# Optimization experiments

Hardware: AMD Instinct MI355X
Metric: run time of the kernel (lower is better)

The kernel has to match this reference:

```python
import jax, jax.numpy as jnp
import numpy as np

N = 100000
E = 1600000
D_IN = 128
D_H = 128
D_OUT = 128
K = 2
EPS = 0.1


def setup_inputs() -> dict:
    key = jax.random.key(0)
    ks = jax.random.split(key, 10)
    x = jax.random.normal(ks[0], (N, D_IN), dtype=jnp.float32)
    edge_index = jax.random.randint(ks[1], (2, E), 0, N, dtype=jnp.int64)
    # parameters (scaled like torch default inits, small uniform)
    def lin(k, fan_in, shape):
        bound = 1.0 / np.sqrt(fan_in)
        return jax.random.uniform(k, shape, jnp.float32, -bound, bound)
    emb_w = lin(ks[2], D_IN, (D_IN, D_H))
    emb_b = lin(ks[3], D_IN, (D_H,))
    # TAGConv: K+1 linears (no bias) + one output bias
    conv_ws = jnp.stack([lin(ks[4 + i], D_H, (D_H, D_H)) for i in range(K + 1)])
    conv_b = lin(ks[7], D_H, (D_H,))
    ro_w = lin(ks[8], D_H, (D_H, D_OUT))
    ro_b = lin(ks[9], D_H, (D_OUT,))
    return {
        "x": x, "edge_index": edge_index, "delta_t": 4,
        "emb_w": emb_w, "emb_b": emb_b,
        "conv_ws": conv_ws, "conv_b": conv_b,
        "ro_w": ro_w, "ro_b": ro_b,
    }


def _tagconv(h, src, dst, norm, conv_ws, conv_b):
    """PyG TAGConv: out = sum_k W_k (A_hat^k h) + b, A_hat = D^-1/2 A D^-1/2 (no self loops)."""
    out = h @ conv_ws[0]
    xk = h
    for k in range(1, K + 1):
        msg = norm[:, None] * xk[src]            # [E, D_H] gather
        xk = jax.ops.segment_sum(msg, dst, num_segments=h.shape[0])  # scatter-add
        out = out + xk @ conv_ws[k]
    return out + conv_b


def reference(x, edge_index, delta_t, emb_w, emb_b, conv_ws, conv_b, ro_w, ro_b):
    src = edge_index[0]
    dst = edge_index[1]
    n = x.shape[0]
    # gcn_norm without self loops: deg over targets of unit edge weights
    deg = jnp.zeros((n,), jnp.float32).at[dst].add(1.0)
    dinv = jnp.where(deg > 0, jax.lax.rsqrt(jnp.maximum(deg, 1.0)), 0.0)
    norm = dinv[src] * dinv[dst]                 # [E]

    h = x @ emb_w + emb_b
    h_middle = h
    for _ in range(int(delta_t)):
        conv = _tagconv(h, src, dst, norm, conv_ws, conv_b)
        h_middle = h + 0.5 * EPS * jnp.tanh(conv)
        conv_mid = _tagconv(h_middle, src, dst, norm, conv_ws, conv_b)
        h = h + EPS * jnp.tanh(conv_mid)
    y = h_middle @ ro_w + ro_b
    return (y, h_middle)
```

## Files before the change

kernel.cpp:

```cpp
#include <hip/hip_runtime.h>
#include <hip/hip_bf16.h>

#define NN 100000
#define EE 1600000
#define DD 128
#define EPSc 0.1f
#define NBK 256
#define BKDIV 391
#define BKCAP 7168

typedef unsigned short bfu;
typedef __attribute__((ext_vector_type(8))) short short8;
typedef __attribute__((ext_vector_type(4))) float f32x4;
typedef __attribute__((ext_vector_type(2))) float f32x2;

__device__ __forceinline__ float bf2f(bfu s) {
    union { unsigned u; float f; } c; c.u = ((unsigned)s) << 16; return c.f;
}
__device__ __forceinline__ bfu f2bf(float f) {
    union { float f; unsigned u; } c; c.f = f;
    unsigned u = c.u + 0x7fffu + ((c.u >> 16) & 1u);
    return (bfu)(u >> 16);
}
__device__ __forceinline__ unsigned pk8(float a, float b, float c, float d) {
    int r = 0;
    r = __builtin_amdgcn_cvt_pk_fp8_f32(a, b, r, false);
    r = __builtin_amdgcn_cvt_pk_fp8_f32(c, d, r, true);
    return (unsigned)r;
}
__device__ __forceinline__ unsigned char enc8(float a) {
    return (unsigned char)(__builtin_amdgcn_cvt_pk_fp8_f32(a, a, 0, false) & 0xFF);
}
__device__ __forceinline__ short8 e8bf(uint2 u) {
    f32x2 p0 = __builtin_amdgcn_cvt_pk_f32_fp8((int)u.x, false);
    f32x2 p1 = __builtin_amdgcn_cvt_pk_f32_fp8((int)u.x, true);
    f32x2 p2 = __builtin_amdgcn_cvt_pk_f32_fp8((int)u.y, false);
    f32x2 p3 = __builtin_amdgcn_cvt_pk_f32_fp8((int)u.y, true);
    short8 s;
    s[0] = (short)f2bf(p0[0]); s[1] = (short)f2bf(p0[1]);
    s[2] = (short)f2bf(p1[0]); s[3] = (short)f2bf(p1[1]);
    s[4] = (short)f2bf(p2[0]); s[5] = (short)f2bf(p2[1]);
    s[6] = (short)f2bf(p3[0]); s[7] = (short)f2bf(p3[1]);
    return s;
}
__device__ __forceinline__ float ftanh(float x) {
    float xc = fminf(fmaxf(x, -9.0f), 9.0f);
    float e = __expf(2.0f * xc);
    return (e - 1.0f) * __builtin_amdgcn_rcpf(e + 1.0f);
}


__global__ __launch_bounds__(256) void count_deg_kernel(const int* __restrict__ dst,
                                                        int* __restrict__ ideg, int e_cnt) {
    int e = blockIdx.x * 256 + threadIdx.x;
    if (e < e_cnt) atomicAdd(&ideg[dst[e]], 1);
}

__global__ __launch_bounds__(256) void dinv_kernel(const int* __restrict__ ideg,
                                                   float* __restrict__ dinv, int n) {
    int i = blockIdx.x * 256 + threadIdx.x;
    if (i < n) {
        int d = ideg[i];
        dinv[i] = (d > 0) ? rsqrtf((float)d) : 0.0f;
    }
}

__global__ __launch_bounds__(256) void partial_sum_kernel(const int* __restrict__ ideg,
                                                          int* __restrict__ partials, int n) {
    __shared__ int sm[256];
    int i = blockIdx.x * 256 + threadIdx.x;
    sm[threadIdx.x] = (i < n) ? ideg[i] : 0;
    __syncthreads();
    for (int off = 128; off > 0; off >>= 1) {
        if ((int)threadIdx.x < off) sm[threadIdx.x] += sm[threadIdx.x + off];
        __syncthreads();
    }
    if (threadIdx.x == 0) partials[blockIdx.x] = sm[0];
}

__global__ __launch_bounds__(512) void scan_partials_kernel(int* __restrict__ partials,
                                                            int* __restrict__ row_ptr,
                                                            int nb, int n) {
    __shared__ int sm[512];
    int v = ((int)threadIdx.x < nb) ? partials[threadIdx.x] : 0;
    sm[threadIdx.x] = v;
    __syncthreads();
    for (int off = 1; off < 512; off <<= 1) {
        int t = (threadIdx.x >= (unsigned)off) ? sm[threadIdx.x - off] : 0;
        __syncthreads();
        sm[threadIdx.x] += t;
        __syncthreads();
    }
    if ((int)threadIdx.x < nb) partials[threadIdx.x] = sm[threadIdx.x] - v;
    if (threadIdx.x == 511) row_ptr[n] = sm[511];
}

__global__ __launch_bounds__(256) void scan_block_kernel(const int* __restrict__ ideg,
                                                         const int* __restrict__ partials,
                                                         int* __restrict__ row_ptr, int n) {
    __shared__ int sm[256];
    int i = blockIdx.x * 256 + threadIdx.x;
    int v = (i < n) ? ideg[i] : 0;
    sm[threadIdx.x] = v;
    __syncthreads();
    for (int off = 1; off < 256; off <<= 1) {
        int t = (threadIdx.x >= (unsigned)off) ? sm[threadIdx.x - off] : 0;
        __syncthreads();
        sm[threadIdx.x] += t;
        __syncthreads();
    }
    if (i < n) row_ptr[i] = partials[blockIdx.x] + sm[threadIdx.x] - v;
}

__global__ __launch_bounds__(256) void bin_kernel(const int* __restrict__ src,
                                                  const int* __restrict__ dst,
                                                  int* __restrict__ bcur,
                                                  uint2* __restrict__ store, int e_cnt) {
    __shared__ int lcnt[NBK];
    __shared__ int lbase[NBK];
    int e0 = blockIdx.x * 4096;
    lcnt[threadIdx.x] = 0;
    __syncthreads();
    for (int k = 0; k < 16; ++k) {
        int e = e0 + k * 256 + (int)threadIdx.x;
        if (e < e_cnt) atomicAdd(&lcnt[(unsigned)dst[e] / BKDIV], 1);
    }
    __syncthreads();
    int c = lcnt[threadIdx.x];
    lbase[threadIdx.x] = (c > 0) ? atomicAdd(&bcur[threadIdx.x], c) : 0;
    __syncthreads();
    lcnt[threadIdx.x] = 0;
    __syncthreads();
    for (int k = 0; k < 16; ++k) {
        int e = e0 + k * 256 + (int)threadIdx.x;
        if (e < e_cnt) {
            int d = dst[e];
            unsigned b = (unsigned)d / BKDIV;
            int p = atomicAdd(&lcnt[b], 1);
            int idx = lbase[b] + p;
            if (idx < BKCAP)
                store[(size_t)b * BKCAP + idx] = make_uint2((unsigned)src[e], (unsigned)d);
        }
    }
}

__global__ __launch_bounds__(256) void place_kernel(const uint2* __restrict__ store,
                                                    const int* __restrict__ bcur,
                                                    const int* __restrict__ row_ptr,
                                                    const float* __restrict__ dinv,
                                                    unsigned* __restrict__ cvp) {
    __shared__ int cur[BKDIV];
    int g = blockIdx.x;
    int d0 = g * BKDIV;
    for (int i = threadIdx.x; i < BKDIV; i += 256) {
        int d = d0 + i;
        cur[i] = (d < NN) ? row_ptr[d] : 0;
    }
    __syncthreads();
    int cnt = bcur[g];
    if (cnt > BKCAP) cnt = BKCAP;
    for (int i = threadIdx.x; i < cnt; i += 256) {
        uint2 w = store[(size_t)g * BKCAP + i];
        int s = (int)w.x, d = (int)w.y;
        int pos = atomicAdd(&cur[d - d0], 1);
        unsigned vb = __float_as_uint(dinv[s] * dinv[d]);
        unsigned r = vb + 0xFFFFu + ((vb >> 17) & 1u);
        cvp[pos] = (r & 0xFFFE0000u) | (unsigned)s;
    }
}


__global__ __launch_bounds__(256) void wfrag_kernel(const float* __restrict__ conv_ws,
                                                    const float* __restrict__ ro_w,
                                                    const float* __restrict__ emb_w,
                                                    bfu* __restrict__ Wf) {
    int m = blockIdx.x;
    const float* W = (m < 3) ? conv_ws + m * 16384 : (m == 3 ? ro_w : emb_w);
    bfu* T = Wf + m * 16384;
    for (int j = 0; j < 64; ++j) {
        int i = threadIdx.x + j * 256;
        int k = i >> 7, n = i & 127;
        int nt = n >> 4, ks = k >> 5, kg = (k >> 3) & 3, jj = k & 7;
        int l = kg * 16 + (n & 15);
        int flat = ((nt * 4 + ks) * 64 + l) * 8 + jj;
        T[flat] = f2bf(W[i]);
    }
}


__device__ __forceinline__ void acc8f8(uint2 u, float v, float* acc) {
    f32x2 p0 = __builtin_amdgcn_cvt_pk_f32_fp8((int)u.x, false);
    f32x2 p1 = __builtin_amdgcn_cvt_pk_f32_fp8((int)u.x, true);
    f32x2 p2 = __builtin_amdgcn_cvt_pk_f32_fp8((int)u.y, false);
    f32x2 p3 = __builtin_amdgcn_cvt_pk_f32_fp8((int)u.y, true);
    acc[0] = fmaf(v, p0[0], acc[0]); acc[1] = fmaf(v, p0[1], acc[1]);
    acc[2] = fmaf(v, p1[0], acc[2]); acc[3] = fmaf(v, p1[1], acc[3]);
    acc[4] = fmaf(v, p2[0], acc[4]); acc[5] = fmaf(v, p2[1], acc[5]);
    acc[6] = fmaf(v, p3[0], acc[6]); acc[7] = fmaf(v, p3[1], acc[7]);
}

__global__ __launch_bounds__(256) void prop_kernel(const unsigned char* __restrict__ xin8,
                                                   unsigned char* __restrict__ out8,
                                                   const int* __restrict__ row_ptr,
                                                   const unsigned* __restrict__ cvp, int n) {
    int wid = (blockIdx.x * 256 + threadIdx.x) >> 6;
    int lane = threadIdx.x & 63;
    if (wid >= n) return;
    int s = row_ptr[wid];
    int deg = row_ptr[wid + 1] - s;
    int g = lane >> 4;
    int li = lane & 15;
    float acc[8] = {0.f, 0.f, 0.f, 0.f, 0.f, 0.f, 0.f, 0.f};
    for (int base = 0; base < deg; base += 64) {
        int cnt = deg - base; if (cnt > 64) cnt = 64;
        unsigned el = (lane < cnt) ? cvp[s + base + lane] : 0u;
        for (int q = 0; q < cnt; q += 16) {
            uint2 x[4]; float v[4];
            #pragma unroll
            for (int j = 0; j < 4; ++j) {
                int idx = q + j * 4 + g;
                unsigned c = __shfl(el, idx);
                bool valid = idx < cnt;
                v[j] = valid ? __uint_as_float(c & 0xFFFE0000u) : 0.f;
                x[j] = valid ? *(const uint2*)(xin8 + (size_t)(c & 0x1FFFFu) * DD + li * 8)
                             : make_uint2(0u, 0u);
            }
            #pragma unroll
            for (int j = 0; j < 4; ++j) acc8f8(x[j], v[j], acc);
        }
    }
    #pragma unroll
    for (int k = 0; k < 8; ++k) {
        acc[k] += __shfl_xor(acc[k], 16);
        acc[k] += __shfl_xor(acc[k], 32);
    }
    if (g == 0) {
        uint2 q;
        q.x = pk8(acc[0], acc[1], acc[2], acc[3]);
        q.y = pk8(acc[4], acc[5], acc[6], acc[7]);
        *(uint2*)(out8 + (size_t)wid * DD + li * 8) = q;
    }
}


template <int NMAT, bool TANH, bool A8, bool RO>
__global__ __launch_bounds__(256) void mfma_mm_kernel(const void* __restrict__ A0,
                                                      const void* __restrict__ A1,
                                                      const void* __restrict__ A2,
                                                      const bfu* __restrict__ Wf,
                                                      const float* __restrict__ bias,
                                                      const bfu* __restrict__ base16,
                                                      float* __restrict__ outf,
                                                      bfu* __restrict__ out16,
                                                      unsigned char* __restrict__ out8,
                                                      const bfu* __restrict__ Wro,
                                                      const float* __restrict__ rob,
                                                      float* __restrict__ yout,
                                                      float scale) {
    int tid = threadIdx.x;
    int wave = tid >> 6, lane = tid & 63;
    int r0 = blockIdx.x * 64 + wave * 16;
    int li = lane & 15, kg = lane >> 4;
    int rowA = r0 + li;
    bool rv = rowA < NN;
    size_t arow = (size_t)(rv ? rowA : 0) * DD;

    const void* As[3] = {A0, A1, A2};
    short8 a[NMAT][4];
    #pragma unroll
    for (int m = 0; m < NMAT; ++m) {
        #pragma unroll
        for (int ks = 0; ks < 4; ++ks) {
            short8 t;
            if (A8) {
                uint2 u = *(const uint2*)((const unsigned char*)As[m] + arow + ks * 32 + kg * 8);
                t = e8bf(u);
            } else {
                t = *(const short8*)((const bfu*)As[m] + arow + ks * 32 + kg * 8);
            }
            if (!rv) t = (short8)0;
            a[m][ks] = t;
        }
    }

    const short8* Bp = (const short8*)Wf;
    f32x4 acc[8];
    #pragma unroll
    for (int nt = 0; nt < 8; ++nt) acc[nt] = (f32x4)(0.f);
    #pragma unroll
    for (int nt = 0; nt < 8; ++nt) {
        #pragma unroll
        for (int m = 0; m < NMAT; ++m) {
            #pragma unroll
            for (int ks = 0; ks < 4; ++ks) {
                short8 b = Bp[m * 2048 + (nt * 4 + ks) * 64 + lane];
                acc[nt] = __builtin_amdgcn_mfma_f32_16x16x32_bf16(a[m][ks], b, acc[nt], 0, 0, 0);
            }
        }
    }

    __shared__ bfu lds_a[RO ? 4 : 1][RO ? 2048 : 1];
    bfu* myt = &lds_a[RO ? wave : 0][0];

    #pragma unroll
    for (int nt = 0; nt < 8; ++nt) {
        int cc = nt * 16 + li;
        float bv = bias[cc];
        #pragma unroll
        for (int rg = 0; rg < 4; ++rg) {
            int rr = r0 + kg * 4 + rg;
            bool v = rr < NN;
            size_t off = (size_t)(v ? rr : 0) * DD + cc;
            float o = acc[nt][rg];
            if (TANH) {
                float ov = v ? (bf2f(base16[off]) + scale * ftanh(o + bv)) : 0.f;
                if (v) {
                    if (outf) outf[off] = ov;
                    if (out16) out16[off] = f2bf(ov);
                    out8[off] = enc8(ov);
                }
                if (RO) {
                    int ks = nt >> 1;
                    int kgk = ((nt & 1) << 1) | (li >> 3);
                    int j = li & 7;
                    int row = kg * 4 + rg;
                    myt[(ks * 64 + kgk * 16 + row) * 8 + j] = f2bf(ov);
                }
            } else {
                if (v) outf[off] = o + bv;
            }
        }
    }

    if (RO) {
        short8 ar[4];
        #pragma unroll
        for (int ks = 0; ks < 4; ++ks)
            ar[ks] = *(const short8*)&myt[(ks * 64 + lane) * 8];
        const short8* Bro = (const short8*)Wro;
        #pragma unroll
        for (int nt = 0; nt < 8; ++nt) {
            f32x4 ay = (f32x4)(0.f);
            #pragma unroll
            for (int ks = 0; ks < 4; ++ks)
                ay = __builtin_amdgcn_mfma_f32_16x16x32_bf16(ar[ks], Bro[(nt * 4 + ks) * 64 + lane], ay, 0, 0, 0);
            int cc = nt * 16 + li;
            float bv = rob[cc];
            #pragma unroll
            for (int rg = 0; rg < 4; ++rg) {
                int rr = r0 + kg * 4 + rg;
                if (rr < NN) yout[(size_t)rr * DD + cc] = ay[rg] + bv;
            }
        }
    }
}


__global__ __launch_bounds__(256) void emb_mfma_kernel(const float* __restrict__ x,
                                                       const bfu* __restrict__ Wfe,
                                                       const float* __restrict__ bias,
                                                       bfu* __restrict__ out16,
                                                       unsigned char* __restrict__ out8) {
    int tid = threadIdx.x;
    int wave = tid >> 6, lane = tid & 63;
    int r0 = blockIdx.x * 64 + wave * 16;
    int li = lane & 15, kg = lane >> 4;
    int rowA = r0 + li;
    bool rv = rowA < NN;
    size_t arow = (size_t)(rv ? rowA : 0) * DD;

    short8 a[4];
    #pragma unroll
    for (int ks = 0; ks < 4; ++ks) {
        const float* px = x + arow + ks * 32 + kg * 8;
        float4 lo = *(const float4*)px;
        float4 hi = *(const float4*)(px + 4);
        short8 t;
        t[0] = (short)f2bf(lo.x); t[1] = (short)f2bf(lo.y);
        t[2] = (short)f2bf(lo.z); t[3] = (short)f2bf(lo.w);
        t[4] = (short)f2bf(hi.x); t[5] = (short)f2bf(hi.y);
        t[6] = (short)f2bf(hi.z); t[7] = (short)f2bf(hi.w);
        if (!rv) t = (short8)0;
        a[ks] = t;
    }

    const short8* Bp = (const short8*)Wfe;
    #pragma unroll
    for (int nt = 0; nt < 8; ++nt) {
        f32x4 acc = (f32x4)(0.f);
        #pragma unroll
        for (int ks = 0; ks < 4; ++ks)
            acc = __builtin_amdgcn_mfma_f32_16x16x32_bf16(a[ks], Bp[(nt * 4 + ks) * 64 + lane], acc, 0, 0, 0);
        int cc = nt * 16 + li;
        float bv = bias[cc];
        #pragma unroll
        for (int rg = 0; rg < 4; ++rg) {
            int rr = r0 + kg * 4 + rg;
            if (rr < NN) {
                size_t off = (size_t)rr * DD + cc;
                float o = acc[rg] + bv;
                out16[off] = f2bf(o);
                out8[off] = enc8(o);
            }
        }
    }
}


extern "C" void kernel_launch(void* const* d_in, const int* in_sizes, int n_in,
                              void* d_out, int out_size, void* d_ws, size_t ws_size,
                              hipStream_t stream) {
    const float* x      = (const float*)d_in[0];
    const int*   eidx   = (const int*)d_in[1];
    const float* emb_w  = (const float*)d_in[3];
    const float* emb_b  = (const float*)d_in[4];
    const float* conv_ws = (const float*)d_in[5];
    const float* conv_b = (const float*)d_in[6];
    const float* ro_w   = (const float*)d_in[7];
    const float* ro_b   = (const float*)d_in[8];

    const int* src = eidx;
    const int* dst = eidx + EE;

    float* y  = (float*)d_out;
    float* hm = y + (size_t)NN * DD;

    char* p = (char*)d_ws;
    const size_t FB2 = (size_t)NN * DD * sizeof(bfu);
    const size_t FB1 = (size_t)NN * DD;
    bfu* h16     = (bfu*)p;                 p += FB2;
    unsigned char* h8  = (unsigned char*)p; p += FB1;
    unsigned char* hm8 = (unsigned char*)p; p += FB1;
    unsigned char* bufA8 = (unsigned char*)p; p += FB1;
    unsigned char* bufB8 = (unsigned char*)p; p += FB1;
    float* dinv  = (float*)p;               p += (size_t)NN * 4;
    int* ideg    = (int*)p;                 p += (size_t)NN * 4;
    int* row_ptr = (int*)p;                 p += (size_t)(NN + 1) * 4;
    int* partials = (int*)p;                p += (size_t)512 * 4;
    int* bcur    = (int*)p;                 p += (size_t)NBK * 4;
    uint2* store = (uint2*)p;               p += (size_t)NBK * BKCAP * 8;
    bfu* Wf      = (bfu*)p;                 p += (size_t)5 * 16384 * sizeof(bfu);
    unsigned* cvp = (unsigned*)p;           p += (size_t)EE * 4;

    const int NB = (NN + 255) / 256;
    const int EB = (EE + 4095) / 4096;

    hipMemsetAsync(ideg, 0, (size_t)NN * 4, stream);
    hipMemsetAsync(bcur, 0, (size_t)NBK * 4, stream);
    count_deg_kernel<<<EE / 256, 256, 0, stream>>>(dst, ideg, EE);
    dinv_kernel<<<NB, 256, 0, stream>>>(ideg, dinv, NN);
    partial_sum_kernel<<<NB, 256, 0, stream>>>(ideg, partials, NN);
    scan_partials_kernel<<<1, 512, 0, stream>>>(partials, row_ptr, NB, NN);
    scan_block_kernel<<<NB, 256, 0, stream>>>(ideg, partials, row_ptr, NN);
    bin_kernel<<<EB, 256, 0, stream>>>(src, dst, bcur, store, EE);
    place_kernel<<<NBK, 256, 0, stream>>>(store, bcur, row_ptr, dinv, cvp);
    wfrag_kernel<<<5, 256, 0, stream>>>(conv_ws, ro_w, emb_w, Wf);

    const int MM_GRID   = (NN + 63) / 64;
    const int PROP_GRID = NN * 64 / 256;

    emb_mfma_kernel<<<MM_GRID, 256, 0, stream>>>(x, Wf + 4 * 16384, emb_b, h16, h8);

    for (int t = 0; t < 4; ++t) {
        prop_kernel<<<PROP_GRID, 256, 0, stream>>>(h8, bufA8, row_ptr, cvp, NN);
        prop_kernel<<<PROP_GRID, 256, 0, stream>>>(bufA8, bufB8, row_ptr, cvp, NN);
        if (t < 3) {
            mfma_mm_kernel<3, true, true, false><<<MM_GRID, 256, 0, stream>>>(
                h8, bufA8, bufB8, Wf, conv_b, h16,
                nullptr, nullptr, hm8, nullptr, nullptr, nullptr, 0.5f * EPSc);

            prop_kernel<<<PROP_GRID, 256, 0, stream>>>(hm8, bufA8, row_ptr, cvp, NN);
            prop_kernel<<<PROP_GRID, 256, 0, stream>>>(bufA8, bufB8, row_ptr, cvp, NN);
            mfma_mm_kernel<3, true, true, false><<<MM_GRID, 256, 0, stream>>>(
                hm8, bufA8, bufB8, Wf, conv_b, h16,
                nullptr, h16, h8, nullptr, nullptr, nullptr, EPSc);
        } else {
            mfma_mm_kernel<3, true, true, true><<<MM_GRID, 256, 0, stream>>>(
                h8, bufA8, bufB8, Wf, conv_b, h16,
                hm, nullptr, hm8, Wf + 3 * 16384, ro_b, y, 0.5f * EPSc);
        }
    }
}
```

Baseline: 1.089 ms.

## Split fp8 feature buffers into two 64-column planes for cache-resident propagation

Stores the fp8 node-feature buffers as two separate 64-column planes instead of a single 128-byte row. Each propagation step now runs as two kernels, one per plane, with 8 lanes per edge and 8 edges per wave-iteration. The goal is a smaller random-gather working set (6.4 MB per plane) that fits better in L2/MALL. The cost is twice as many prop launches and a second pass over row_ptr and edge metadata. The matmul kernels read and write the planar layout through updated address arithmetic.

```diff
diff --git a/kernel.cpp b/kernel.cpp
--- a/kernel.cpp
+++ b/kernel.cpp
@@ -8,6 +8,7 @@
 #define NBK 256
 #define BKDIV 391
 #define BKCAP 7168
+#define PL ((size_t)NN * 64)
 
 typedef unsigned short bfu;
 typedef __attribute__((ext_vector_type(8))) short short8;
@@ -208,21 +209,21 @@
     if (wid >= n) return;
     int s = row_ptr[wid];
     int deg = row_ptr[wid + 1] - s;
-    int g = lane >> 4;
-    int li = lane & 15;
+    int g = lane >> 3;
+    int li = lane & 7;
     float acc[8] = {0.f, 0.f, 0.f, 0.f, 0.f, 0.f, 0.f, 0.f};
     for (int base = 0; base < deg; base += 64) {
         int cnt = deg - base; if (cnt > 64) cnt = 64;
         unsigned el = (lane < cnt) ? cvp[s + base + lane] : 0u;
-        for (int q = 0; q < cnt; q += 16) {
+        for (int q = 0; q < cnt; q += 32) {
             uint2 x[4]; float v[4];
             #pragma unroll
             for (int j = 0; j < 4; ++j) {
-                int idx = q + j * 4 + g;
+                int idx = q + j * 8 + g;
                 unsigned c = __shfl(el, idx);
                 bool valid = idx < cnt;
                 v[j] = valid ? __uint_as_float(c & 0xFFFE0000u) : 0.f;
-                x[j] = valid ? *(const uint2*)(xin8 + (size_t)(c & 0x1FFFFu) * DD + li * 8)
+                x[j] = valid ? *(const uint2*)(xin8 + (size_t)(c & 0x1FFFFu) * 64 + li * 8)
                              : make_uint2(0u, 0u);
             }
             #pragma unroll
@@ -231,6 +232,7 @@
     }
     #pragma unroll
     for (int k = 0; k < 8; ++k) {
+        acc[k] += __shfl_xor(acc[k], 8);
         acc[k] += __shfl_xor(acc[k], 16);
         acc[k] += __shfl_xor(acc[k], 32);
     }
@@ -238,15 +240,15 @@
         uint2 q;
         q.x = pk8(acc[0], acc[1], acc[2], acc[3]);
         q.y = pk8(acc[4], acc[5], acc[6], acc[7]);
-        *(uint2*)(out8 + (size_t)wid * DD + li * 8) = q;
-    }
-}
-
-
-template <int NMAT, bool TANH, bool A8, bool RO>
-__global__ __launch_bounds__(256) void mfma_mm_kernel(const void* __restrict__ A0,
-                                                      const void* __restrict__ A1,
-                                                      const void* __restrict__ A2,
+        *(uint2*)(out8 + (size_t)wid * 64 + li * 8) = q;
+    }
+}
+
+
+template <int NMAT, bool TANH, bool RO>
+__global__ __launch_bounds__(256) void mfma_mm_kernel(const unsigned char* __restrict__ A0,
+                                                      const unsigned char* __restrict__ A1,
+                                                      const unsigned char* __restrict__ A2,
                                                       const bfu* __restrict__ Wf,
                                                       const float* __restrict__ bias,
                                                       const bfu* __restrict__ base16,
@@ -263,21 +265,16 @@
     int li = lane & 15, kg = lane >> 4;
     int rowA = r0 + li;
     bool rv = rowA < NN;
-    size_t arow = (size_t)(rv ? rowA : 0) * DD;
-
-    const void* As[3] = {A0, A1, A2};
+    size_t arow = (size_t)(rv ? rowA : 0) * 64;
+
+    const unsigned char* As[3] = {A0, A1, A2};
     short8 a[NMAT][4];
     #pragma unroll
     for (int m = 0; m < NMAT; ++m) {
         #pragma unroll
         for (int ks = 0; ks < 4; ++ks) {
-            short8 t;
-            if (A8) {
-                uint2 u = *(const uint2*)((const unsigned char*)As[m] + arow + ks * 32 + kg * 8);
-                t = e8bf(u);
-            } else {
-                t = *(const short8*)((const bfu*)As[m] + arow + ks * 32 + kg * 8);
-            }
+            uint2 u = *(const uint2*)(As[m] + (size_t)(ks >> 1) * PL + arow + (ks & 1) * 32 + kg * 8);
+            short8 t = e8bf(u);
             if (!rv) t = (short8)0;
             a[m][ks] = t;
         }
@@ -317,7 +314,7 @@
                 if (v) {
                     if (outf) outf[off] = ov;
                     if (out16) out16[off] = f2bf(ov);
-                    out8[off] = enc8(ov);
+                    out8[(size_t)(nt >> 2) * PL + (size_t)rr * 64 + ((nt & 3) * 16 + li)] = enc8(ov);
                 }
                 if (RO) {
                     int ks = nt >> 1;
@@ -400,7 +397,7 @@
                 size_t off = (size_t)rr * DD + cc;
                 float o = acc[rg] + bv;
                 out16[off] = f2bf(o);
-                out8[off] = enc8(o);
+                out8[(size_t)(nt >> 2) * PL + (size_t)rr * 64 + ((nt & 3) * 16 + li)] = enc8(o);
             }
         }
     }
@@ -427,12 +424,11 @@
 
     char* p = (char*)d_ws;
     const size_t FB2 = (size_t)NN * DD * sizeof(bfu);
-    const size_t FB1 = (size_t)NN * DD;
     bfu* h16     = (bfu*)p;                 p += FB2;
-    unsigned char* h8  = (unsigned char*)p; p += FB1;
-    unsigned char* hm8 = (unsigned char*)p; p += FB1;
-    unsigned char* bufA8 = (unsigned char*)p; p += FB1;
-    unsigned char* bufB8 = (unsigned char*)p; p += FB1;
+    unsigned char* h8  = (unsigned char*)p; p += 2 * PL;
+    unsigned char* hm8 = (unsigned char*)p; p += 2 * PL;
+    unsigned char* bufA8 = (unsigned char*)p; p += 2 * PL;
+    unsigned char* bufB8 = (unsigned char*)p; p += 2 * PL;
     float* dinv  = (float*)p;               p += (size_t)NN * 4;
     int* ideg    = (int*)p;                 p += (size_t)NN * 4;
     int* row_ptr = (int*)p;                 p += (size_t)(NN + 1) * 4;
@@ -462,20 +458,24 @@
     emb_mfma_kernel<<<MM_GRID, 256, 0, stream>>>(x, Wf + 4 * 16384, emb_b, h16, h8);
 
     for (int t = 0; t < 4; ++t) {
-        prop_kernel<<<PROP_GRID, 256, 0, stream>>>(h8, bufA8, row_ptr, cvp, NN);
-        prop_kernel<<<PROP_GRID, 256, 0, stream>>>(bufA8, bufB8, row_ptr, cvp, NN);
+        for (int pl = 0; pl < 2; ++pl) {
+            prop_kernel<<<PROP_GRID, 256, 0, stream>>>(h8 + pl * PL, bufA8 + pl * PL, row_ptr, cvp, NN);
+            prop_kernel<<<PROP_GRID, 256, 0, stream>>>(bufA8 + pl * PL, bufB8 + pl * PL, row_ptr, cvp, NN);
+        }
         if (t < 3) {
-            mfma_mm_kernel<3, true, true, false><<<MM_GRID, 256, 0, stream>>>(
+            mfma_mm_kernel<3, true, false><<<MM_GRID, 256, 0, stream>>>(
                 h8, bufA8, bufB8, Wf, conv_b, h16,
                 nullptr, nullptr, hm8, nullptr, nullptr, nullptr, 0.5f * EPSc);
 
-            prop_kernel<<<PROP_GRID, 256, 0, stream>>>(hm8, bufA8, row_ptr, cvp, NN);
-            prop_kernel<<<PROP_GRID, 256, 0, stream>>>(bufA8, bufB8, row_ptr, cvp, NN);
-            mfma_mm_kernel<3, true, true, false><<<MM_GRID, 256, 0, stream>>>(
+            for (int pl = 0; pl < 2; ++pl) {
+                prop_kernel<<<PROP_GRID, 256, 0, stream>>>(hm8 + pl * PL, bufA8 + pl * PL, row_ptr, cvp, NN);
+                prop_kernel<<<PROP_GRID, 256, 0, stream>>>(bufA8 + pl * PL, bufB8 + pl * PL, row_ptr, cvp, NN);
+            }
+            mfma_mm_kernel<3, true, false><<<MM_GRID, 256, 0, stream>>>(
                 hm8, bufA8, bufB8, Wf, conv_b, h16,
                 nullptr, h16, h8, nullptr, nullptr, nullptr, EPSc);
         } else {
-            mfma_mm_kernel<3, true, true, true><<<MM_GRID, 256, 0, stream>>>(
+            mfma_mm_kernel<3, true, true><<<MM_GRID, 256, 0, stream>>>(
                 h8, bufA8, bufB8, Wf, conv_b, h16,
                 hm, nullptr, hm8, Wf + 3 * 16384, ro_b, y, 0.5f * EPSc);
         }
```

Result: slower. 1.485 ms (+36.3%).
